# Kernel tuning notes

Hardware: AMD Instinct MI355X
Metric: run time of the kernel (lower is better)

The kernel has to match this reference:

```python
import jax, jax.numpy as jnp
import numpy as np

B, N, H, D, DEPTH = 16, 1024, 2, 128, 3
A = H * D  # atten_dim = 256
FFN = 1024
EPS = 1e-5


def layer_norm(x, g, b):
    mu = jnp.mean(x, axis=-1, keepdims=True)
    var = jnp.mean(jnp.square(x - mu), axis=-1, keepdims=True)
    return (x - mu) * jax.lax.rsqrt(var + EPS) * g + b


def setup_inputs() -> dict:
    key = jax.random.key(0)
    ks = jax.random.split(key, 16)
    s = lambda fan_in: 1.0 / np.sqrt(fan_in)
    inp = {
        "X": jax.random.normal(ks[0], (B, N, A), jnp.float32),
        # per-layer attention projections, stacked over depth
        "Wq": jax.random.normal(ks[1], (DEPTH, A, A), jnp.float32) * s(A),
        "bq": jnp.zeros((DEPTH, A), jnp.float32),
        "Wk": jax.random.normal(ks[2], (DEPTH, A, A), jnp.float32) * s(A),
        "bk": jnp.zeros((DEPTH, A), jnp.float32),
        "Wv": jax.random.normal(ks[3], (DEPTH, A, A), jnp.float32) * s(A),
        "bv": jnp.zeros((DEPTH, A), jnp.float32),
        # per-layer FFN (roll_out): Linear(A,1024)+ReLU, Linear(1024,A)+ReLU
        "W1": jax.random.normal(ks[4], (DEPTH, A, FFN), jnp.float32) * s(A),
        "b1": jnp.zeros((DEPTH, FFN), jnp.float32),
        "W2": jax.random.normal(ks[5], (DEPTH, FFN, A), jnp.float32) * s(FFN),
        "b2": jnp.zeros((DEPTH, A), jnp.float32),
        # single shared LayerNorm (the torch module reuses one instance)
        "ln_g": jnp.ones((A,), jnp.float32),
        "ln_b": jnp.zeros((A,), jnp.float32),
        # Conv1d(A, A, kernel_size=1) == per-position linear over channels
        "Wc": jax.random.normal(ks[6], (A, A), jnp.float32) * s(A),
        "bc": jnp.zeros((A,), jnp.float32),
        # final Linear(A, A) on pooled features
        "We": jax.random.normal(ks[7], (A, A), jnp.float32) * s(A),
        "be": jnp.zeros((A,), jnp.float32),
    }
    return inp


def reference(X, Wq, bq, Wk, bk, Wv, bv, W1, b1, W2, b2, ln_g, ln_b, Wc, bc, We, be):
    inv_sqrt_d = 1.0 / np.sqrt(D)
    step = X  # [B, N, A]
    for i in range(DEPTH):
        q = (step @ Wq[i] + bq[i]).reshape(B, N, H, D).transpose(0, 2, 1, 3)
        k = (step @ Wk[i] + bk[i]).reshape(B, N, H, D).transpose(0, 2, 1, 3)
        v = (step @ Wv[i] + bv[i]).reshape(B, N, H, D).transpose(0, 2, 1, 3)
        scores = jnp.einsum('bhqd,bhkd->bhqk', q, k) * inv_sqrt_d
        probs = jax.nn.softmax(scores, axis=-1)
        attn = jnp.einsum('bhqk,bhkd->bhqd', probs, v)
        attn = attn.transpose(0, 2, 1, 3).reshape(B, N, A)
        roll = jax.nn.relu(jax.nn.relu(attn @ W1[i] + b1[i]) @ W2[i] + b2[i])
        step = layer_norm(roll + step, ln_g, ln_b)
    # Conv1d(kernel=1) + ReLU over channels, per position
    entity_encodings = jax.nn.relu(step @ Wc + bc)  # [B, N, A]
    pooled = jnp.mean(entity_encodings, axis=1)      # [B, A]
    encoded_entities = jax.nn.relu(pooled @ We + be)  # [B, A]
    return encoded_entities
```

## Files before the change

### kernel.cpp

```cpp
#include <hip/hip_runtime.h>
#include <hip/hip_bf16.h>
#include <cstddef>

#define B_   16
#define N_   1024
#define H_   2
#define D_   128
#define A_   256
#define FFN_ 1024
#define M_   (B_ * N_)
#define EPS_ 1e-5f
#define SPLIT 4
#define KT   32
#define TPC  (N_ / SPLIT / KT)
#define QKV_E ((size_t)B_ * H_ * N_ * D_)

typedef short  short8  __attribute__((ext_vector_type(8)));
typedef float  f32x16  __attribute__((ext_vector_type(16)));
typedef unsigned int uint;
typedef unsigned short ushort;

#define MFMA32(a, b, c) __builtin_amdgcn_mfma_f32_32x32x16_bf16(a, b, c, 0, 0, 0)

__device__ __forceinline__ uint f2b1(float x) {
    uint u = __float_as_uint(x);
    return (u + 0x7fffu + ((u >> 16) & 1u)) >> 16;
}
__device__ __forceinline__ uint f2b2(float lo, float hi) {
    return f2b1(lo) | (f2b1(hi) << 16);
}
__device__ __forceinline__ float b2f(ushort u) {
    return __uint_as_float(((uint)u) << 16);
}

__global__ __launch_bounds__(256) void f32_to_bf16_kernel(
    const float* __restrict__ in, ushort* __restrict__ out)
{
    const size_t i = ((size_t)blockIdx.x * 256 + threadIdx.x) * 8;
    float4 a = *(const float4*)(in + i);
    float4 b = *(const float4*)(in + i + 4);
    uint4 w = { f2b2(a.x, a.y), f2b2(a.z, a.w), f2b2(b.x, b.y), f2b2(b.z, b.w) };
    *(uint4*)(out + i) = w;
}

__global__ __launch_bounds__(256) void prep_kernel(
    const float* __restrict__ Wq, const float* __restrict__ Wk,
    const float* __restrict__ Wv, const float* __restrict__ W1,
    const float* __restrict__ W2, const float* __restrict__ Wc,
    ushort* __restrict__ wqkv_t, ushort* __restrict__ w1_t,
    ushort* __restrict__ w2_t, ushort* __restrict__ wc_t)
{
    const int z = blockIdx.z;
    const float* W; ushort* out; int K, N, n0, k0;
    if (z < 9) {
        const int layer = z / 3, sec = z % 3;
        W = (sec == 0 ? Wq : sec == 1 ? Wk : Wv) + (size_t)layer * A_ * A_;
        out = wqkv_t + (size_t)layer * 3 * A_ * A_ + (size_t)sec * A_ * A_;
        K = A_; N = A_;
        n0 = blockIdx.x * 32; k0 = blockIdx.y * 32;
    } else if (z < 12) {
        const int layer = z - 9;
        W = W1 + (size_t)layer * A_ * FFN_; out = w1_t + (size_t)layer * A_ * FFN_;
        K = A_; N = FFN_;
        n0 = blockIdx.x * 32; k0 = blockIdx.y * 32;
    } else if (z < 15) {
        const int layer = z - 12;
        W = W2 + (size_t)layer * FFN_ * A_; out = w2_t + (size_t)layer * FFN_ * A_;
        K = FFN_; N = A_;
        k0 = blockIdx.x * 32; n0 = blockIdx.y * 32;
    } else {
        W = Wc; out = wc_t; K = A_; N = A_;
        n0 = blockIdx.x * 32; k0 = blockIdx.y * 32;
    }
    if (n0 >= N || k0 >= K) return;

    __shared__ float tile[32][33];
    const int tc = threadIdx.x & 31, tr = threadIdx.x >> 5;
#pragma unroll
    for (int it = 0; it < 4; ++it) {
        int r = it * 8 + tr;
        tile[r][tc] = W[(size_t)(k0 + r) * N + n0 + tc];
    }
    __syncthreads();
#pragma unroll
    for (int it = 0; it < 4; ++it) {
        int r = it * 8 + tr;
        out[(size_t)(n0 + r) * K + k0 + tc] = (ushort)f2b1(tile[tc][r]);
    }
}

template <int MR>
__global__ __launch_bounds__(256) void gemm_mfma(
    const ushort* __restrict__ Asrc, const ushort* __restrict__ Wt,
    const float* __restrict__ bias, const float* __restrict__ biasK,
    const float* __restrict__ biasV, void* __restrict__ outp,
    int K, int ldc, int mode)
{
    constexpr int BM = MR * 64;
    __shared__ ushort sA[BM * 72];
    __shared__ ushort sB[128 * 72];

    const int tid = threadIdx.x;
    const int wid = tid >> 6, lane = tid & 63;
    const int c = lane & 31, g = lane >> 5;
    const int wr = wid >> 1, wc = wid & 1;
    const int m0 = blockIdx.x * BM;
    const int n0 = blockIdx.y * 128;

    f32x16 acc[MR][2] = {};

    for (int k0 = 0; k0 < K; k0 += 64) {
        __syncthreads();
#pragma unroll
        for (int it = 0; it < BM / 32; ++it) {
            int idx = it * 256 + tid, r = idx >> 3, cc = (idx & 7) * 8;
            *(uint4*)&sA[r * 72 + cc] =
                *(const uint4*)(Asrc + (size_t)(m0 + r) * K + k0 + cc);
        }
#pragma unroll
        for (int it = 0; it < 4; ++it) {
            int idx = it * 256 + tid, r = idx >> 3, cc = (idx & 7) * 8;
            *(uint4*)&sB[r * 72 + cc] =
                *(const uint4*)(Wt + (size_t)(n0 + r) * K + k0 + cc);
        }
        __syncthreads();
#pragma unroll
        for (int ks = 0; ks < 4; ++ks) {
            const int ko = ks * 16 + 8 * g;
            short8 b0 = *(const short8*)&sB[(wc * 64 + c) * 72 + ko];
            short8 b1 = *(const short8*)&sB[(wc * 64 + 32 + c) * 72 + ko];
#pragma unroll
            for (int mr = 0; mr < MR; ++mr) {
                short8 a = *(const short8*)&sA[((wr * MR + mr) * 32 + c) * 72 + ko];
                acc[mr][0] = MFMA32(a, b0, acc[mr][0]);
                acc[mr][1] = MFMA32(a, b1, acc[mr][1]);
            }
        }
    }

    const int sec = n0 >> 8;
    const float* bp = bias;
    int nw = n0;
    if (mode == 5) {
        bp = (sec == 0 ? bias : sec == 1 ? biasK : biasV);
        nw = n0 & 255;
    }
    const float bz[2] = { bp[nw + wc * 64 + c], bp[nw + wc * 64 + 32 + c] };

    float colsum[2] = { 0.f, 0.f };

#pragma unroll
    for (int mr = 0; mr < MR; ++mr) {
#pragma unroll
        for (int ct = 0; ct < 2; ++ct) {
            const int colbase = n0 + wc * 64 + ct * 32 + c;
#pragma unroll
            for (int rg = 0; rg < 4; ++rg) {
                const int row = m0 + (wr * MR + mr) * 32 + 8 * rg + 4 * g;
                float v0 = acc[mr][ct][4 * rg + 0] + bz[ct];
                float v1 = acc[mr][ct][4 * rg + 1] + bz[ct];
                float v2 = acc[mr][ct][4 * rg + 2] + bz[ct];
                float v3 = acc[mr][ct][4 * rg + 3] + bz[ct];
                if (mode == 1 || mode == 2 || mode == 6) {
                    v0 = fmaxf(v0, 0.f); v1 = fmaxf(v1, 0.f);
                    v2 = fmaxf(v2, 0.f); v3 = fmaxf(v3, 0.f);
                }
                if (mode == 1) {
                    float* o = (float*)outp;
                    o[(size_t)(row + 0) * ldc + colbase] = v0;
                    o[(size_t)(row + 1) * ldc + colbase] = v1;
                    o[(size_t)(row + 2) * ldc + colbase] = v2;
                    o[(size_t)(row + 3) * ldc + colbase] = v3;
                } else if (mode == 2) {
                    ushort* o = (ushort*)outp;
                    o[(size_t)(row + 0) * ldc + colbase] = (ushort)f2b1(v0);
                    o[(size_t)(row + 1) * ldc + colbase] = (ushort)f2b1(v1);
                    o[(size_t)(row + 2) * ldc + colbase] = (ushort)f2b1(v2);
                    o[(size_t)(row + 3) * ldc + colbase] = (ushort)f2b1(v3);
                } else if (mode == 6) {
                    colsum[ct] += v0 + v1 + v2 + v3;
                } else {
                    const int cw = colbase & 255;
                    const int hh = cw >> 7, dd = cw & (D_ - 1);
                    if (sec < 2) {
                        ushort* o = (ushort*)outp + (size_t)sec * QKV_E;
#pragma unroll
                        for (int r2 = 0; r2 < 4; ++r2) {
                            int rw = row + r2;
                            int bb = rw >> 10, np = rw & (N_ - 1);
                            float vv = (r2 == 0 ? v0 : r2 == 1 ? v1 : r2 == 2 ? v2 : v3);
                            size_t off = (((size_t)(bb * H_ + hh) * 32 + (np >> 5)) * 16
                                          + (dd >> 3)) * 256
                                         + (np & 31) * 8 + (dd & 7);
                            o[off] = (ushort)f2b1(vv);
                        }
                    } else {
                        ushort* o = (ushort*)outp + 2 * QKV_E;
                        const int bb = row >> 10, np = row & (N_ - 1);
                        size_t off = ((((size_t)(bb * H_ + hh) * 32 + (np >> 5)) * 4
                                       + (dd >> 5)) * 4 + ((np & 31) >> 3)) * 256
                                     + (dd & 31) * 8 + (np & 7);
                        uint2 w = { f2b2(v0, v1), f2b2(v2, v3) };
                        *(uint2*)(o + off) = w;
                    }
                }
            }
        }
    }

    if (mode == 6) {
        float* part = (float*)outp;
        const int b = m0 >> 10;
#pragma unroll
        for (int ct = 0; ct < 2; ++ct) {
            float cs = colsum[ct] + __shfl_xor(colsum[ct], 32, 64);
            if (g == 0)
                atomicAdd(&part[(size_t)b * A_ + n0 + wc * 64 + ct * 32 + c], cs);
        }
    }
}

#define OPITCH 132

__global__ __launch_bounds__(128, 2) void attn_kernel(
    const ushort* __restrict__ qg, const ushort* __restrict__ kg,
    const ushort* __restrict__ vtg, ushort* __restrict__ po,
    float* __restrict__ pm, float* __restrict__ pl)
{
    __shared__ ushort sO[64 * OPITCH];

    const int tid = threadIdx.x;
    const int w = tid >> 6, lane = tid & 63;
    const int c = lane & 31, g = lane >> 5;

    const int flat = blockIdx.x;
    const int xcd  = flat & 7;
    const int ii   = flat >> 3;
    const int pair = xcd * 16 + (ii & 15);
    const int qt   = ii >> 4;
    const int bh   = pair & 31;
    const int z    = pair >> 5;

    const int q0 = qt * 64 + w * 32;
    const float scale2 = 0.08838834764831845f * 1.44269504f;
    const float THR = 11.5f;
    const int lo8 = c * 8;

    short8 qf[8];
    const ushort* qt_ = qg + ((size_t)bh * 32 + (q0 >> 5)) * 4096;
#pragma unroll
    for (int ks = 0; ks < 8; ++ks)
        qf[ks] = *(const short8*)(qt_ + (2 * ks + g) * 256 + lo8);

    f32x16 oacc[4] = {};
    float m = -1e30f, l = 0.f;

    const size_t chunk0 = ((size_t)bh * 32 + z * 8) * 4096;
    const ushort* kb0 = kg + chunk0 + g * 256 + lo8;
    short8 kf0 = *(const short8*)(kb0 + 0 * 512);
    short8 kf1 = *(const short8*)(kb0 + 1 * 512);
    short8 kf2 = *(const short8*)(kb0 + 2 * 512);
    short8 kf3 = *(const short8*)(kb0 + 3 * 512);
    short8 kf4 = *(const short8*)(kb0 + 4 * 512);
    short8 kf5 = *(const short8*)(kb0 + 5 * 512);
    short8 kf6 = *(const short8*)(kb0 + 6 * 512);
    short8 kf7 = *(const short8*)(kb0 + 7 * 512);

    for (int t = 0; t < TPC; ++t) {
        const size_t tb = chunk0 + (size_t)t * 4096;

        const ushort* vb = vtg + tb + g * 256 + lo8;
        short8 vfA0 = *(const short8*)(vb + 0 * 1024);
        short8 vfA1 = *(const short8*)(vb + 1 * 1024);
        short8 vfA2 = *(const short8*)(vb + 2 * 1024);
        short8 vfA3 = *(const short8*)(vb + 3 * 1024);
        short8 vfB0 = *(const short8*)(vb + 0 * 1024 + 512);
        short8 vfB1 = *(const short8*)(vb + 1 * 1024 + 512);
        short8 vfB2 = *(const short8*)(vb + 2 * 1024 + 512);
        short8 vfB3 = *(const short8*)(vb + 3 * 1024 + 512);
        __builtin_amdgcn_sched_barrier(0);

        f32x16 sacc = {};
        __builtin_amdgcn_s_setprio(1);
        sacc = MFMA32(kf0, qf[0], sacc);
        sacc = MFMA32(kf1, qf[1], sacc);
        sacc = MFMA32(kf2, qf[2], sacc);
        sacc = MFMA32(kf3, qf[3], sacc);
        sacc = MFMA32(kf4, qf[4], sacc);
        sacc = MFMA32(kf5, qf[5], sacc);
        sacc = MFMA32(kf6, qf[6], sacc);
        sacc = MFMA32(kf7, qf[7], sacc);
        __builtin_amdgcn_s_setprio(0);

        if (t + 1 < TPC) {
            const ushort* kb2 = kg + tb + 4096 + g * 256 + lo8;
            kf0 = *(const short8*)(kb2 + 0 * 512);
            kf1 = *(const short8*)(kb2 + 1 * 512);
            kf2 = *(const short8*)(kb2 + 2 * 512);
            kf3 = *(const short8*)(kb2 + 3 * 512);
            kf4 = *(const short8*)(kb2 + 4 * 512);
            kf5 = *(const short8*)(kb2 + 5 * 512);
            kf6 = *(const short8*)(kb2 + 6 * 512);
            kf7 = *(const short8*)(kb2 + 7 * 512);
        }
        __builtin_amdgcn_sched_barrier(0);

        float p[16];
        float tmax = -1e30f;
#pragma unroll
        for (int r = 0; r < 16; ++r) {
            float s = sacc[r] * scale2;
            p[r] = s;
            tmax = fmaxf(tmax, s);
        }
        tmax = fmaxf(tmax, __shfl_xor(tmax, 32, 64));
        if (!__all(tmax - m <= THR)) {
            const float mnew = fmaxf(m, tmax);
            const float corr = exp2f(m - mnew);
#pragma unroll
            for (int dt = 0; dt < 4; ++dt)
#pragma unroll
                for (int r = 0; r < 16; ++r) oacc[dt][r] *= corr;
            l *= corr;
            m = mnew;
        }
        float tsum = 0.f;
#pragma unroll
        for (int r = 0; r < 16; ++r) {
            p[r] = exp2f(p[r] - m);
            tsum += p[r];
        }
        tsum += __shfl_xor(tsum, 32, 64);
        l += tsum;

        uint pk[8];
#pragma unroll
        for (int pp = 0; pp < 8; ++pp)
            pk[pp] = f2b2(p[2 * pp], p[2 * pp + 1]);

        uint v0 = g ? pk[0] : pk[2];
        uint v1 = g ? pk[1] : pk[3];
        uint v2 = g ? pk[4] : pk[6];
        uint v3 = g ? pk[5] : pk[7];
        uint r0 = (uint)__shfl_xor((int)v0, 32, 64);
        uint r1 = (uint)__shfl_xor((int)v1, 32, 64);
        uint r2 = (uint)__shfl_xor((int)v2, 32, 64);
        uint r3 = (uint)__shfl_xor((int)v3, 32, 64);

        __builtin_amdgcn_s_setprio(1);
#pragma unroll
        for (int kb = 0; kb < 2; ++kb) {
            union { uint u[4]; short8 s; } pf;
            if (kb == 0) {
                pf.u[0] = g ? r0 : pk[0];
                pf.u[1] = g ? r1 : pk[1];
                pf.u[2] = g ? pk[2] : r0;
                pf.u[3] = g ? pk[3] : r1;
            } else {
                pf.u[0] = g ? r2 : pk[4];
                pf.u[1] = g ? r3 : pk[5];
                pf.u[2] = g ? pk[6] : r2;
                pf.u[3] = g ? pk[7] : r3;
            }
            oacc[0] = MFMA32(kb ? vfB0 : vfA0, pf.s, oacc[0]);
            oacc[1] = MFMA32(kb ? vfB1 : vfA1, pf.s, oacc[1]);
            oacc[2] = MFMA32(kb ? vfB2 : vfA2, pf.s, oacc[2]);
            oacc[3] = MFMA32(kb ? vfB3 : vfA3, pf.s, oacc[3]);
        }
        __builtin_amdgcn_s_setprio(0);
    }

    if (lane < 32) {
        pm[(size_t)(z * 32 + bh) * N_ + q0 + c] = m;
        pl[(size_t)(z * 32 + bh) * N_ + q0 + c] = l;
    }
    {
        const int qrl = w * 32 + c;
#pragma unroll
        for (int dt = 0; dt < 4; ++dt)
#pragma unroll
            for (int rg = 0; rg < 4; ++rg) {
                int d = dt * 32 + 8 * rg + 4 * g;
                uint2 pv = { f2b2(oacc[dt][4 * rg + 0], oacc[dt][4 * rg + 1]),
                             f2b2(oacc[dt][4 * rg + 2], oacc[dt][4 * rg + 3]) };
                *(uint2*)&sO[qrl * OPITCH + d] = pv;
            }
    }
    __syncthreads();
    {
        const size_t pbase = ((size_t)(z * 32 + bh) * N_ + qt * 64) * D_;
#pragma unroll
        for (int it = 0; it < 16; ++it) {
            int idx = it * 128 + tid;
            int r = idx >> 5, dgr = (idx & 31) * 4;
            uint2 v = *(const uint2*)&sO[r * OPITCH + dgr];
            *(uint2*)(po + pbase + (size_t)r * D_ + dgr) = v;
        }
    }
}

__global__ __launch_bounds__(256) void combine_kernel(
    const ushort* __restrict__ po, const float* __restrict__ pm,
    const float* __restrict__ pl, ushort* __restrict__ out)
{
    const int idx = blockIdx.x * 256 + threadIdx.x;
    const int row = idx >> 4, d0 = (idx & 15) * 8;
    const int R = B_ * H_ * N_;

    float ms[SPLIT];
    float M = -1e30f;
#pragma unroll
    for (int s = 0; s < SPLIT; ++s) {
        ms[s] = pm[(size_t)s * R + row];
        M = fmaxf(M, ms[s]);
    }
    float L = 0.f;
    float acc[8] = {};
#pragma unroll
    for (int s = 0; s < SPLIT; ++s) {
        float wgt = exp2f(ms[s] - M);
        L += pl[(size_t)s * R + row] * wgt;
        uint4 pv = *(const uint4*)(po + ((size_t)s * R + row) * D_ + d0);
        const ushort* pu = (const ushort*)&pv;
#pragma unroll
        for (int j = 0; j < 8; ++j) acc[j] += b2f(pu[j]) * wgt;
    }
    const float inv = 1.f / L;
    uint4 w;
    w.x = f2b2(acc[0] * inv, acc[1] * inv);
    w.y = f2b2(acc[2] * inv, acc[3] * inv);
    w.z = f2b2(acc[4] * inv, acc[5] * inv);
    w.w = f2b2(acc[6] * inv, acc[7] * inv);
    const int bh = row >> 10, n = row & (N_ - 1);
    const int bb = bh >> 1, hh = bh & 1;
    *(uint4*)(out + ((size_t)(bb * N_ + n)) * A_ + hh * D_ + d0) = w;
}

__global__ __launch_bounds__(256) void add_ln_kernel(
    const ushort* __restrict__ roll, ushort* __restrict__ stepb,
    const float* __restrict__ g, const float* __restrict__ bta)
{
    const int row = blockIdx.x * 4 + (threadIdx.x >> 6);
    const int lane = threadIdx.x & 63, c4 = lane * 4;
    const size_t base = (size_t)row * A_ + c4;

    uint2 rb = *(const uint2*)(roll + base);
    uint2 pb = *(const uint2*)(stepb + base);
    float v0 = b2f((ushort)(rb.x & 0xffff)) + b2f((ushort)(pb.x & 0xffff));
    float v1 = b2f((ushort)(rb.x >> 16))    + b2f((ushort)(pb.x >> 16));
    float v2 = b2f((ushort)(rb.y & 0xffff)) + b2f((ushort)(pb.y & 0xffff));
    float v3 = b2f((ushort)(rb.y >> 16))    + b2f((ushort)(pb.y >> 16));

    float s  = v0 + v1 + v2 + v3;
    float s2 = v0 * v0 + v1 * v1 + v2 * v2 + v3 * v3;
#pragma unroll
    for (int o = 32; o > 0; o >>= 1) {
        s  += __shfl_xor(s, o, 64);
        s2 += __shfl_xor(s2, o, 64);
    }
    const float mu = s * (1.f / A_);
    const float rs = rsqrtf(s2 * (1.f / A_) - mu * mu + EPS_);

    float4 gv = *(const float4*)(g + c4);
    float4 bv = *(const float4*)(bta + c4);
    float y0 = (v0 - mu) * rs * gv.x + bv.x;
    float y1 = (v1 - mu) * rs * gv.y + bv.y;
    float y2 = (v2 - mu) * rs * gv.z + bv.z;
    float y3 = (v3 - mu) * rs * gv.w + bv.w;

    uint2 yb = { f2b2(y0, y1), f2b2(y2, y3) };
    *(uint2*)(stepb + base) = yb;
}

__global__ __launch_bounds__(256) void final_kernel(
    const float* __restrict__ part, const float* __restrict__ We,
    const float* __restrict__ be, float* __restrict__ out)
{
    __shared__ float sp[A_];
    const int b = blockIdx.x, tid = threadIdx.x;
    sp[tid] = part[(size_t)b * A_ + tid] * (1.0f / N_);
    __syncthreads();
    float acc = be[tid];
    for (int kk = 0; kk < A_; ++kk) acc += sp[kk] * We[(size_t)kk * A_ + tid];
    out[b * A_ + tid] = fmaxf(acc, 0.f);
}

extern "C" void kernel_launch(void* const* d_in, const int* in_sizes, int n_in,
                              void* d_out, int out_size, void* d_ws, size_t ws_size,
                              hipStream_t stream)
{
    const float* X    = (const float*)d_in[0];
    const float* Wq   = (const float*)d_in[1];
    const float* bq   = (const float*)d_in[2];
    const float* Wk   = (const float*)d_in[3];
    const float* bk   = (const float*)d_in[4];
    const float* Wv   = (const float*)d_in[5];
    const float* bv   = (const float*)d_in[6];
    const float* W1   = (const float*)d_in[7];
    const float* b1   = (const float*)d_in[8];
    const float* W2   = (const float*)d_in[9];
    const float* b2   = (const float*)d_in[10];
    const float* ln_g = (const float*)d_in[11];
    const float* ln_b = (const float*)d_in[12];
    const float* Wc   = (const float*)d_in[13];
    const float* bc   = (const float*)d_in[14];
    const float* We   = (const float*)d_in[15];
    const float* be   = (const float*)d_in[16];

    char* base = (char*)d_ws;
    ushort* qb     = (ushort*)base;  base += QKV_E * 2;
                             base += QKV_E * 2;
                             base += QKV_E * 2;
    ushort* hbuf   = (ushort*)base;  base += (size_t)M_ * FFN_ * 2;
    ushort* rollb  = (ushort*)base;  base += (size_t)M_ * A_ * 2;
    ushort* stepb  = (ushort*)base;  base += (size_t)M_ * A_ * 2;
    ushort* wqkv_t = (ushort*)base;  base += (size_t)3 * 3 * A_ * A_ * 2;
    ushort* w1_t   = (ushort*)base;  base += (size_t)3 * A_ * FFN_ * 2;
    ushort* w2_t   = (ushort*)base;  base += (size_t)3 * FFN_ * A_ * 2;
    ushort* wc_t   = (ushort*)base;  base += (size_t)A_ * A_ * 2;
    float*  part   = (float*)base;   base += (size_t)B_ * A_ * 4;
    float*  pm     = (float*)base;   base += (size_t)SPLIT * B_ * H_ * N_ * 4;
    float*  pl     = (float*)base;   base += (size_t)SPLIT * B_ * H_ * N_ * 4;
    ushort* kbuf   = qb + QKV_E;
    ushort* vtbuf  = qb + 2 * QKV_E;
    ushort* po     = hbuf;
    ushort* attnb  = qb;

    prep_kernel<<<dim3(32, 8, 16), 256, 0, stream>>>(
        Wq, Wk, Wv, W1, W2, Wc, wqkv_t, w1_t, w2_t, wc_t);
    f32_to_bf16_kernel<<<(M_ * A_) / (256 * 8), 256, 0, stream>>>(X, stepb);

    for (int i = 0; i < 3; ++i) {
        gemm_mfma<2><<<dim3(M_/128, 6), 256, 0, stream>>>(
            stepb, wqkv_t + (size_t)i * 3 * A_ * A_,
            bq + i * A_, bk + i * A_, bv + i * A_, qb, A_, 0, 5);

        attn_kernel<<<16 * SPLIT * B_ * H_, 128, 0, stream>>>(
            qb, kbuf, vtbuf, po, pm, pl);
        combine_kernel<<<(B_*H_*N_*D_)/(256*8), 256, 0, stream>>>(po, pm, pl, attnb);

        gemm_mfma<2><<<dim3(M_/128, FFN_/128), 256, 0, stream>>>(
            attnb, w1_t + (size_t)i * A_ * FFN_, b1 + i * FFN_, nullptr, nullptr,
            hbuf, A_, FFN_, 2);
        gemm_mfma<1><<<dim3(M_/64, A_/128), 256, 0, stream>>>(
            hbuf, w2_t + (size_t)i * FFN_ * A_, b2 + i * A_, nullptr, nullptr,
            rollb, FFN_, A_, 2);

        add_ln_kernel<<<M_/4, 256, 0, stream>>>(rollb, stepb, ln_g, ln_b);
    }

    hipMemsetAsync(part, 0, (size_t)B_ * A_ * 4, stream);
    gemm_mfma<1><<<dim3(M_/64, A_/128), 256, 0, stream>>>(
        stepb, wc_t, bc, nullptr, nullptr, part, A_, 0, 6);
    final_kernel<<<B_, 256, 0, stream>>>(part, We, be, (float*)d_out);
}
```

Measured before the change: 365.6 us.

## Fuse split-KV attention combine into FFN1 GEMM A-load and halve split count

Removes the separate combine kernel by merging the partial attention outputs (rescaled by the per-split max and sum) while loading A tiles in the first FFN GEMM. The KV split factor also drops from 4 to 2, which halves the attention grid and the partial-output traffic but gives each block a longer loop. Buffers are re-laid out so the partial outputs get their own region. The mode-8 combine is hardcoded for exactly two splits, and every FFN1 block that shares the same rows redoes the exp and divide work.

```diff
diff --git a/kernel.cpp b/kernel.cpp
--- a/kernel.cpp
+++ b/kernel.cpp
@@ -10,7 +10,7 @@
 #define FFN_ 1024
 #define M_   (B_ * N_)
 #define EPS_ 1e-5f
-#define SPLIT 4
+#define SPLIT 2
 #define KT   32
 #define TPC  (N_ / SPLIT / KT)
 #define QKV_E ((size_t)B_ * H_ * N_ * D_)
@@ -94,7 +94,7 @@
     const ushort* __restrict__ Asrc, const ushort* __restrict__ Wt,
     const float* __restrict__ bias, const float* __restrict__ biasK,
     const float* __restrict__ biasV, void* __restrict__ outp,
-    int K, int ldc, int mode)
+    int Kloop, int lda, int ldc, int mode)
 {
     constexpr int BM = MR * 64;
     __shared__ ushort sA[BM * 72];
@@ -109,19 +109,49 @@
 
     f32x16 acc[MR][2] = {};
 
-    for (int k0 = 0; k0 < K; k0 += 64) {
+    for (int k0 = 0; k0 < Kloop; k0 += 64) {
         __syncthreads();
-#pragma unroll
-        for (int it = 0; it < BM / 32; ++it) {
-            int idx = it * 256 + tid, r = idx >> 3, cc = (idx & 7) * 8;
-            *(uint4*)&sA[r * 72 + cc] =
-                *(const uint4*)(Asrc + (size_t)(m0 + r) * K + k0 + cc);
+        if (mode == 8) {
+#pragma unroll
+            for (int it = 0; it < BM / 32; ++it) {
+                int idx = it * 256 + tid, r = idx >> 3, cc = (idx & 7) * 8;
+                const int row = m0 + r;
+                const int bb2 = row >> 10, nn = row & (N_ - 1);
+                const int col = k0 + cc;
+                const int hh = col >> 7, d0 = col & (D_ - 1);
+                const int pr = (((bb2 << 1) | hh) << 10) + nn;
+                const float ms0 = biasK[pr], ms1 = biasK[32 * N_ + pr];
+                const float Mx = fmaxf(ms0, ms1);
+                const float w0 = exp2f(ms0 - Mx), w1 = exp2f(ms1 - Mx);
+                const float invL = 1.f / (biasV[pr] * w0 + biasV[32 * N_ + pr] * w1);
+                const float f0 = w0 * invL, f1 = w1 * invL;
+                uint4 pa = *(const uint4*)(Asrc + (size_t)pr * D_ + d0);
+                uint4 pb = *(const uint4*)(Asrc + QKV_E + (size_t)pr * D_ + d0);
+                const ushort* pua = (const ushort*)&pa;
+                const ushort* pub = (const ushort*)&pb;
+                uint4 wv;
+                uint* wp = (uint*)&wv;
+#pragma unroll
+                for (int j = 0; j < 4; ++j) {
+                    float e0 = b2f(pua[2 * j])     * f0 + b2f(pub[2 * j])     * f1;
+                    float e1 = b2f(pua[2 * j + 1]) * f0 + b2f(pub[2 * j + 1]) * f1;
+                    wp[j] = f2b2(e0, e1);
+                }
+                *(uint4*)&sA[r * 72 + cc] = wv;
+            }
+        } else {
+#pragma unroll
+            for (int it = 0; it < BM / 32; ++it) {
+                int idx = it * 256 + tid, r = idx >> 3, cc = (idx & 7) * 8;
+                *(uint4*)&sA[r * 72 + cc] =
+                    *(const uint4*)(Asrc + (size_t)(m0 + r) * lda + k0 + cc);
+            }
         }
 #pragma unroll
         for (int it = 0; it < 4; ++it) {
             int idx = it * 256 + tid, r = idx >> 3, cc = (idx & 7) * 8;
             *(uint4*)&sB[r * 72 + cc] =
-                *(const uint4*)(Wt + (size_t)(n0 + r) * K + k0 + cc);
+                *(const uint4*)(Wt + (size_t)(n0 + r) * lda + k0 + cc);
         }
         __syncthreads();
 #pragma unroll
@@ -161,7 +191,7 @@
                 float v1 = acc[mr][ct][4 * rg + 1] + bz[ct];
                 float v2 = acc[mr][ct][4 * rg + 2] + bz[ct];
                 float v3 = acc[mr][ct][4 * rg + 3] + bz[ct];
-                if (mode == 1 || mode == 2 || mode == 6) {
+                if (mode == 1 || mode == 2 || mode == 6 || mode == 8) {
                     v0 = fmaxf(v0, 0.f); v1 = fmaxf(v1, 0.f);
                     v2 = fmaxf(v2, 0.f); v3 = fmaxf(v3, 0.f);
                 }
@@ -171,7 +201,7 @@
                     o[(size_t)(row + 1) * ldc + colbase] = v1;
                     o[(size_t)(row + 2) * ldc + colbase] = v2;
                     o[(size_t)(row + 3) * ldc + colbase] = v3;
-                } else if (mode == 2) {
+                } else if (mode == 2 || mode == 8) {
                     ushort* o = (ushort*)outp;
                     o[(size_t)(row + 0) * ldc + colbase] = (ushort)f2b1(v0);
                     o[(size_t)(row + 1) * ldc + colbase] = (ushort)f2b1(v1);
@@ -236,8 +266,8 @@
     const int flat = blockIdx.x;
     const int xcd  = flat & 7;
     const int ii   = flat >> 3;
-    const int pair = xcd * 16 + (ii & 15);
-    const int qt   = ii >> 4;
+    const int pair = xcd * 8 + (ii & 7);
+    const int qt   = ii >> 3;
     const int bh   = pair & 31;
     const int z    = pair >> 5;
 
@@ -255,7 +285,7 @@
     f32x16 oacc[4] = {};
     float m = -1e30f, l = 0.f;
 
-    const size_t chunk0 = ((size_t)bh * 32 + z * 8) * 4096;
+    const size_t chunk0 = ((size_t)bh * 32 + z * TPC) * 4096;
     const ushort* kb0 = kg + chunk0 + g * 256 + lo8;
     short8 kf0 = *(const short8*)(kb0 + 0 * 512);
     short8 kf1 = *(const short8*)(kb0 + 1 * 512);
@@ -399,43 +429,6 @@
     }
 }
 
-__global__ __launch_bounds__(256) void combine_kernel(
-    const ushort* __restrict__ po, const float* __restrict__ pm,
-    const float* __restrict__ pl, ushort* __restrict__ out)
-{
-    const int idx = blockIdx.x * 256 + threadIdx.x;
-    const int row = idx >> 4, d0 = (idx & 15) * 8;
-    const int R = B_ * H_ * N_;
-
-    float ms[SPLIT];
-    float M = -1e30f;
-#pragma unroll
-    for (int s = 0; s < SPLIT; ++s) {
-        ms[s] = pm[(size_t)s * R + row];
-        M = fmaxf(M, ms[s]);
-    }
-    float L = 0.f;
-    float acc[8] = {};
-#pragma unroll
-    for (int s = 0; s < SPLIT; ++s) {
-        float wgt = exp2f(ms[s] - M);
-        L += pl[(size_t)s * R + row] * wgt;
-        uint4 pv = *(const uint4*)(po + ((size_t)s * R + row) * D_ + d0);
-        const ushort* pu = (const ushort*)&pv;
-#pragma unroll
-        for (int j = 0; j < 8; ++j) acc[j] += b2f(pu[j]) * wgt;
-    }
-    const float inv = 1.f / L;
-    uint4 w;
-    w.x = f2b2(acc[0] * inv, acc[1] * inv);
-    w.y = f2b2(acc[2] * inv, acc[3] * inv);
-    w.z = f2b2(acc[4] * inv, acc[5] * inv);
-    w.w = f2b2(acc[6] * inv, acc[7] * inv);
-    const int bh = row >> 10, n = row & (N_ - 1);
-    const int bb = bh >> 1, hh = bh & 1;
-    *(uint4*)(out + ((size_t)(bb * N_ + n)) * A_ + hh * D_ + d0) = w;
-}
-
 __global__ __launch_bounds__(256) void add_ln_kernel(
     const ushort* __restrict__ roll, ushort* __restrict__ stepb,
     const float* __restrict__ g, const float* __restrict__ bta)
@@ -508,10 +501,8 @@
     const float* be   = (const float*)d_in[16];
 
     char* base = (char*)d_ws;
-    ushort* qb     = (ushort*)base;  base += QKV_E * 2;
-                             base += QKV_E * 2;
-                             base += QKV_E * 2;
-    ushort* hbuf   = (ushort*)base;  base += (size_t)M_ * FFN_ * 2;
+    ushort* fbuf   = (ushort*)base;  base += (size_t)M_ * FFN_ * 2;
+    ushort* po     = (ushort*)base;  base += (size_t)SPLIT * QKV_E * 2;
     ushort* rollb  = (ushort*)base;  base += (size_t)M_ * A_ * 2;
     ushort* stepb  = (ushort*)base;  base += (size_t)M_ * A_ * 2;
     ushort* wqkv_t = (ushort*)base;  base += (size_t)3 * 3 * A_ * A_ * 2;
@@ -521,10 +512,9 @@
     float*  part   = (float*)base;   base += (size_t)B_ * A_ * 4;
     float*  pm     = (float*)base;   base += (size_t)SPLIT * B_ * H_ * N_ * 4;
     float*  pl     = (float*)base;   base += (size_t)SPLIT * B_ * H_ * N_ * 4;
-    ushort* kbuf   = qb + QKV_E;
-    ushort* vtbuf  = qb + 2 * QKV_E;
-    ushort* po     = hbuf;
-    ushort* attnb  = qb;
+    ushort* qb     = fbuf;
+    ushort* kbuf   = fbuf + QKV_E;
+    ushort* vtbuf  = fbuf + 2 * QKV_E;
 
     prep_kernel<<<dim3(32, 8, 16), 256, 0, stream>>>(
         Wq, Wk, Wv, W1, W2, Wc, wqkv_t, w1_t, w2_t, wc_t);
@@ -533,24 +523,24 @@
     for (int i = 0; i < 3; ++i) {
         gemm_mfma<2><<<dim3(M_/128, 6), 256, 0, stream>>>(
             stepb, wqkv_t + (size_t)i * 3 * A_ * A_,
-            bq + i * A_, bk + i * A_, bv + i * A_, qb, A_, 0, 5);
+            bq + i * A_, bk + i * A_, bv + i * A_, qb, A_, A_, 0, 5);
 
         attn_kernel<<<16 * SPLIT * B_ * H_, 128, 0, stream>>>(
             qb, kbuf, vtbuf, po, pm, pl);
-        combine_kernel<<<(B_*H_*N_*D_)/(256*8), 256, 0, stream>>>(po, pm, pl, attnb);
 
         gemm_mfma<2><<<dim3(M_/128, FFN_/128), 256, 0, stream>>>(
-            attnb, w1_t + (size_t)i * A_ * FFN_, b1 + i * FFN_, nullptr, nullptr,
-            hbuf, A_, FFN_, 2);
+            po, w1_t + (size_t)i * A_ * FFN_, b1 + i * FFN_, pm, pl,
+            fbuf, A_, A_, FFN_, 8);
+
         gemm_mfma<1><<<dim3(M_/64, A_/128), 256, 0, stream>>>(
-            hbuf, w2_t + (size_t)i * FFN_ * A_, b2 + i * A_, nullptr, nullptr,
-            rollb, FFN_, A_, 2);
+            fbuf, w2_t + (size_t)i * FFN_ * A_, b2 + i * A_, nullptr, nullptr,
+            rollb, FFN_, FFN_, A_, 2);
 
         add_ln_kernel<<<M_/4, 256, 0, stream>>>(rollb, stepb, ln_g, ln_b);
     }
 
     hipMemsetAsync(part, 0, (size_t)B_ * A_ * 4, stream);
     gemm_mfma<1><<<dim3(M_/64, A_/128), 256, 0, stream>>>(
-        stepb, wc_t, bc, nullptr, nullptr, part, A_, 0, 6);
+        stepb, wc_t, bc, nullptr, nullptr, part, A_, A_, 0, 6);
     final_kernel<<<B_, 256, 0, stream>>>(part, We, be, (float*)d_out);
 }
```

Result: no change. 367.7 us (+0.6%).
